# Kernel optimization log

Hardware: AMD Instinct MI355X
Metric: run time of the kernel (lower is better)

Reference implementation:

```python
import jax, jax.numpy as jnp
import numpy as np

EPS = 1e-5

def _ln(x, w, b, axes):
    mu = jnp.mean(x, axis=axes, keepdims=True)
    var = jnp.mean((x - mu) ** 2, axis=axes, keepdims=True)
    return (x - mu) / jnp.sqrt(var + EPS) * w + b

def setup_inputs() -> dict:
    key = jax.random.key(0)
    ks = jax.random.split(key, 6)
    B, L, D, A, H, F = 1, 1024, 512, 32, 8, 2048
    s = 0.02
    return {
        "x": jax.random.normal(ks[0], (B, L, D), jnp.float32),
        "ln0_w": jnp.ones((D,), jnp.float32),
        "ln0_b": jnp.zeros((D,), jnp.float32),
        "ln1_w": jnp.ones((D, H), jnp.float32),
        "ln1_b": jnp.zeros((D, H), jnp.float32),
        "qw": jax.random.normal(ks[1], (D, A * H), jnp.float32) * s,
        "qb": jnp.zeros((A * H,), jnp.float32),
        "kw": jax.random.normal(ks[2], (D, A * H), jnp.float32) * s,
        "kb": jnp.zeros((A * H,), jnp.float32),
        "vw": jax.random.normal(ks[3], (D, D * H), jnp.float32) * s,
        "vb": jnp.zeros((D * H,), jnp.float32),
        "w1": jax.random.normal(ks[4], (D * H, F), jnp.float32) * s,
        "b1": jnp.zeros((F,), jnp.float32),
        "w2": jax.random.normal(ks[5], (F, D), jnp.float32) * s,
        "b2": jnp.zeros((D,), jnp.float32),
    }

def reference(x, ln0_w, ln0_b, ln1_w, ln1_b, qw, qb, kw, kb, vw, vb, w1, b1, w2, b2):
    B, L, D = x.shape
    H = ln1_w.shape[-1]
    _x = _ln(x, ln0_w, ln0_b, -1)
    # q, k: [B, L, d_att, H] with exp(clamp(.)) feature map
    q = jnp.exp(jnp.clip(_x @ qw + qb, -10.0, 10.0)).reshape(B, L, -1, H)
    k = jnp.exp(jnp.clip(_x @ kw + kb, -10.0, 10.0)).reshape(B, L, -1, H)
    # v uses raw x (not layernormed): [B, L, D, H]
    v = (x @ vw + vb).reshape(B, L, D, H)
    # cumulative outer-product KV state: [B, L, d_att, D, H]
    kv = jnp.cumsum(jnp.einsum('blah,bldh->bladh', k, v), axis=1)
    qkv = jnp.einsum('blah,bladh->bldh', q, kv)          # [B, L, D, H]
    den = jnp.einsum('blah,blah->blh', q, jnp.cumsum(k, axis=1))[..., None, :]  # [B, L, 1, H]
    y = x[..., None] + _ln(qkv / den, ln1_w, ln1_b, (-2, -1))  # LN over (D, H) jointly
    y = y.reshape(B, L, D * H)
    h1 = jax.nn.relu(y @ w1 + b1)
    return jax.nn.relu(h1 @ w2 + b2) + x
```

## Files before the change

kernel.cpp:

```cpp
#include <hip/hip_runtime.h>
#include <hip/hip_bf16.h>
#include <math.h>

#define L_SEQ 1024
#define D_DIM 512
#define A_DIM 32
#define H_DIM 8
#define F_DIM 2048
#define AH 256
#define DH 4096
#define NC 16
#define CH 64
#define EPS_LN 1e-5f

typedef __attribute__((ext_vector_type(8))) short short8;
typedef __attribute__((ext_vector_type(4))) short short4v;
typedef __attribute__((ext_vector_type(2))) short short2v;
typedef __attribute__((ext_vector_type(4))) float floatx4;

#define ASYNC_COPY16(gp, lp)                                                     \
    __builtin_amdgcn_global_load_lds(                                            \
        (const __attribute__((address_space(1))) void*)(const void*)(gp),        \
        (__attribute__((address_space(3))) void*)(void*)(lp), 16, 0, 0)

__global__ __launch_bounds__(256) void prep_kernel(const float* __restrict__ x,
                                                   const float* __restrict__ ln0w,
                                                   const float* __restrict__ ln0b,
                                                   const float* __restrict__ ln1w,
                                                   const float* __restrict__ ln1b,
                                                   const float* __restrict__ qw,
                                                   const float* __restrict__ kw,
                                                   const float* __restrict__ vw,
                                                   const float* __restrict__ w1,
                                                   const float* __restrict__ w2,
                                                   __hip_bfloat16* __restrict__ xn,
                                                   __hip_bfloat16* __restrict__ xb,
                                                   __hip_bfloat16* __restrict__ qkwt,
                                                   __hip_bfloat16* __restrict__ vwt,
                                                   __hip_bfloat16* __restrict__ w1t,
                                                   __hip_bfloat16* __restrict__ w2t,
                                                   float* __restrict__ wp,
                                                   float* __restrict__ bp) {
    __shared__ float tt[32][33];
    __shared__ float red[8];
    int bid = blockIdx.x;
    int tid = threadIdx.x;
    if (bid < 1024) {
        int l = bid;
        float v0 = x[l * D_DIM + tid];
        float v1 = x[l * D_DIM + 256 + tid];
        float s = v0 + v1, s2 = v0 * v0 + v1 * v1;
        for (int off = 32; off > 0; off >>= 1) {
            s += __shfl_down(s, off);
            s2 += __shfl_down(s2, off);
        }
        int lane = tid & 63, wid = tid >> 6;
        if (lane == 0) { red[wid] = s; red[4 + wid] = s2; }
        __syncthreads();
        float ts = red[0] + red[1] + red[2] + red[3];
        float t2 = red[4] + red[5] + red[6] + red[7];
        float mu = ts / (float)D_DIM;
        float var = t2 / (float)D_DIM - mu * mu;
        float rs = rsqrtf(var + EPS_LN);
        xn[l * D_DIM + tid]       = (__hip_bfloat16)((v0 - mu) * rs * ln0w[tid] + ln0b[tid]);
        xn[l * D_DIM + 256 + tid] = (__hip_bfloat16)((v1 - mu) * rs * ln0w[256 + tid] + ln0b[256 + tid]);
        xb[l * D_DIM + tid]       = (__hip_bfloat16)v0;
        xb[l * D_DIM + 256 + tid] = (__hip_bfloat16)v1;
        return;
    }
    if (bid == 12544) {
        int e0 = tid * 16;
        float o1[16], o2[16];
#pragma unroll
        for (int j = 0; j < 16; ++j) {
            int ee = e0 + j;
            int pi = ((ee & 511) << 3) | (ee >> 9);
            o1[j] = ln1w[pi];
            o2[j] = ln1b[pi];
        }
#pragma unroll
        for (int j = 0; j < 4; ++j) {
            *(float4*)(wp + e0 + j * 4) = *(float4*)&o1[j * 4];
            *(float4*)(bp + e0 + j * 4) = *(float4*)&o2[j * 4];
        }
        return;
    }
    const float* in;
    __hip_bfloat16* out;
    int R, C, mode = 0, t;
    if (bid < 1152)      { t = bid - 1024;  in = qw; out = qkwt;                      R = 512;  C = 256; }
    else if (bid < 1280) { t = bid - 1152;  in = kw; out = qkwt + (size_t)AH * D_DIM; R = 512;  C = 256; }
    else if (bid < 3328) { t = bid - 1280;  in = vw; out = vwt;  mode = 1;            R = 512;  C = 4096; }
    else if (bid < 11520){ t = bid - 3328;  in = w1; out = w1t;  mode = 2;            R = 4096; C = 2048; }
    else                 { t = bid - 11520; in = w2; out = w2t;                       R = 2048; C = 512; }
    int ctiles = C >> 5;
    int cx = t % ctiles, cy = t / ctiles;
    int r0 = cy * 32, c0 = cx * 32;
    {
        int r_in = tid >> 3, c4 = (tid & 7) * 4;
        int rr = r0 + r_in;
        if (mode == 2) rr = ((rr & 511) << 3) | (rr >> 9);
        float4 v = *(const float4*)(in + (size_t)rr * C + c0 + c4);
        tt[r_in][c4 + 0] = v.x;
        tt[r_in][c4 + 1] = v.y;
        tt[r_in][c4 + 2] = v.z;
        tt[r_in][c4 + 3] = v.w;
    }
    __syncthreads();
    {
        int c_out = tid >> 3, r4 = (tid & 7) * 4;
        int c = c0 + c_out;
        int orow = (mode == 1) ? (((c & 7) << 9) | (c >> 3)) : c;
        __hip_bfloat16 o[4];
#pragma unroll
        for (int j = 0; j < 4; ++j) o[j] = (__hip_bfloat16)tt[r4 + j][c_out];
        *(short4v*)(out + (size_t)orow * R + r0 + r4) = *(short4v*)o;
    }
}

template <int BN>
__device__ __forceinline__ void gemm_core(const __hip_bfloat16* __restrict__ A,
                                          const __hip_bfloat16* __restrict__ Bt,
                                          int K, int bm, int bn, int k_beg, int k_end,
                                          __hip_bfloat16* As, __hip_bfloat16* Bs,
                                          floatx4 (&acc)[2][BN / 32]) {
    constexpr int NT = BN / 32;
    const int tid = threadIdx.x;
    const int w = tid >> 6, lane = tid & 63;
    const int wm = (w >> 1) * 32, wn = (w & 1) * (BN / 2);
    const int quad = lane >> 4, l16 = lane & 15;
    const int srow = tid >> 4, sslot = tid & 15;
    const int scg = sslot ^ srow;
    for (int k0 = k_beg; k0 < k_end; k0 += 128) {
        __syncthreads();
#pragma unroll
        for (int j = 0; j < 4; ++j)
            ASYNC_COPY16(A + (size_t)(bm + j * 16 + srow) * K + k0 + scg * 8,
                         As + j * 2048 + w * 512);
#pragma unroll
        for (int j = 0; j < BN / 16; ++j)
            ASYNC_COPY16(Bt + (size_t)(bn + j * 16 + srow) * K + k0 + scg * 8,
                         Bs + j * 2048 + w * 512);
        __syncthreads();
#pragma unroll
        for (int ks = 0; ks < 4; ++ks) {
            short8 af[2], bfr[NT];
#pragma unroll
            for (int mt = 0; mt < 2; ++mt) {
                int rr = wm + mt * 16 + l16;
                af[mt] = *(const short8*)(As + rr * 128 + (((ks * 4 + quad) ^ (rr & 15)) * 8));
            }
#pragma unroll
            for (int nt = 0; nt < NT; ++nt) {
                int rr = wn + nt * 16 + l16;
                bfr[nt] = *(const short8*)(Bs + rr * 128 + (((ks * 4 + quad) ^ (rr & 15)) * 8));
            }
#pragma unroll
            for (int mt = 0; mt < 2; ++mt)
#pragma unroll
                for (int nt = 0; nt < NT; ++nt)
                    acc[mt][nt] = __builtin_amdgcn_mfma_f32_16x16x32_bf16(
                        af[mt], bfr[nt], acc[mt][nt], 0, 0, 0);
        }
    }
}

__global__ __launch_bounds__(256) void qkv_gemm(const __hip_bfloat16* __restrict__ xn,
                                                const __hip_bfloat16* __restrict__ xb,
                                                const __hip_bfloat16* __restrict__ qkwt,
                                                const __hip_bfloat16* __restrict__ vwt,
                                                const float* __restrict__ qb,
                                                const float* __restrict__ kb,
                                                const float* __restrict__ vb,
                                                __hip_bfloat16* __restrict__ q2,
                                                __hip_bfloat16* __restrict__ k2,
                                                __hip_bfloat16* __restrict__ vT) {
    __shared__ __align__(16) __hip_bfloat16 As[64 * 128];
    __shared__ __align__(16) __hip_bfloat16 Bs[64 * 128];
    const int tid = threadIdx.x;
    const int w = tid >> 6, lane = tid & 63;
    const int wm = (w >> 1) * 32, wn = (w & 1) * 32;
    const int quad = lane >> 4, l16 = lane & 15;
    int bid = blockIdx.x;
    bool isv = bid < 1024;
    const __hip_bfloat16 *A, *Bt;
    int bx, by;
    if (isv) {
        int r = bid >> 3;
        bx = (bid & 7) * 8 + (r & 7);
        by = r >> 3;
        A = xb; Bt = vwt;
    } else {
        int b2 = bid - 1024;
        bx = b2 & 7; by = b2 >> 3;
        A = xn; Bt = qkwt;
    }
    const int bm = by * 64, bn = bx * 64;
    floatx4 acc[2][2];
#pragma unroll
    for (int i = 0; i < 2; ++i)
#pragma unroll
        for (int j = 0; j < 2; ++j) acc[i][j] = (floatx4)0.f;
    gemm_core<64>(A, Bt, D_DIM, bm, bn, 0, D_DIM, As, Bs, acc);
    if (isv) {
        __syncthreads();
        __hip_bfloat16* Ct = As;
#pragma unroll
        for (int mt = 0; mt < 2; ++mt)
#pragma unroll
            for (int nt = 0; nt < 2; ++nt) {
                int col = bn + wn + nt * 16 + l16;
                int bi = ((col & 511) << 3) | (col >> 9);
                float bbv = vb[bi];
                __hip_bfloat16 tmp[4];
#pragma unroll
                for (int r = 0; r < 4; ++r)
                    tmp[r] = (__hip_bfloat16)(acc[mt][nt][r] + bbv);
                *(short4v*)&Ct[(wn + nt * 16 + l16) * 72 + wm + mt * 16 + quad * 4] =
                    *(short4v*)tmp;
            }
        __syncthreads();
        int colloc = tid >> 2, seg = (tid & 3) * 16;
        short8 o0 = *(const short8*)&Ct[colloc * 72 + seg];
        short8 o1 = *(const short8*)&Ct[colloc * 72 + seg + 8];
        *(short8*)(vT + (size_t)(bn + colloc) * 1024 + bm + seg) = o0;
        *(short8*)(vT + (size_t)(bn + colloc) * 1024 + bm + seg + 8) = o1;
    } else {
        __syncthreads();
        __hip_bfloat16* q2t = As;
        bool isq = bn < 256;
        const float* bias = isq ? qb : kb;
        int cb = isq ? bn : bn - 256;
#pragma unroll
        for (int mt = 0; mt < 2; ++mt)
#pragma unroll
            for (int nt = 0; nt < 2; ++nt) {
                int colloc = wn + nt * 16 + l16;
                float bb = bias[cb + colloc];
                int hh = colloc & 7, aa = colloc >> 3;
#pragma unroll
                for (int r = 0; r < 4; ++r) {
                    int rowloc = wm + mt * 16 + quad * 4 + r;
                    float val = expf(fminf(fmaxf(acc[mt][nt][r] + bb, -10.f), 10.f));
                    q2t[((hh * 64 + rowloc) << 3) + aa] = (__hip_bfloat16)val;
                }
            }
        __syncthreads();
        __hip_bfloat16* dst = isq ? q2 : k2;
        int a0 = cb >> 3;
#pragma unroll
        for (int j = 0; j < 2; ++j) {
            int p = tid + j * 256;
            int hh = p >> 6, ll = p & 63;
            short8 o = *(const short8*)&q2t[(hh * 64 + ll) << 3];
            *(short8*)(dst + (size_t)(hh * 1024 + bm + ll) * 32 + a0) = o;
        }
    }
}

__global__ __launch_bounds__(256) void w1_gemm(const __hip_bfloat16* __restrict__ y,
                                               const __hip_bfloat16* __restrict__ w1t,
                                               const float* __restrict__ b1,
                                               __hip_bfloat16* __restrict__ h1) {
    __shared__ __align__(16) __hip_bfloat16 As[64 * 128];
    __shared__ __align__(16) __hip_bfloat16 Bs[32 * 128];
    const int tid = threadIdx.x;
    const int w = tid >> 6, lane = tid & 63;
    const int wm = (w >> 1) * 32, wn = (w & 1) * 16;
    const int quad = lane >> 4, l16 = lane & 15;
    int bid = blockIdx.x;
    int r = bid >> 3;
    int bx = (bid & 7) * 8 + (r & 7);
    int by = r >> 3;
    const int bm = by * 64, bn = bx * 32;
    floatx4 acc[2][1];
    acc[0][0] = (floatx4)0.f;
    acc[1][0] = (floatx4)0.f;
    gemm_core<32>(y, w1t, DH, bm, bn, 0, DH, As, Bs, acc);
    int col = bn + wn + l16;
    float bb = b1[col];
#pragma unroll
    for (int mt = 0; mt < 2; ++mt)
#pragma unroll
        for (int rr = 0; rr < 4; ++rr) {
            int row = bm + wm + mt * 16 + quad * 4 + rr;
            h1[(size_t)row * F_DIM + col] =
                (__hip_bfloat16)fmaxf(acc[mt][0][rr] + bb, 0.f);
        }
}

template <int STRIP>
__global__ __launch_bounds__(256) void gemm_split(const __hip_bfloat16* __restrict__ A,
                                                  const __hip_bfloat16* __restrict__ Bt,
                                                  float* __restrict__ part,
                                                  int M, int N, int K, int Ksub) {
    __shared__ __align__(16) __hip_bfloat16 As[64 * 128];
    __shared__ __align__(16) __hip_bfloat16 Bs[64 * 128];
    const int tid = threadIdx.x;
    const int w = tid >> 6, lane = tid & 63;
    const int wm = (w >> 1) * 32, wn = (w & 1) * 32;
    const int quad = lane >> 4, l16 = lane & 15;
    int bid = blockIdx.x;
    int r = bid >> 3;
    int bx = (bid & 7) * STRIP + (r % STRIP);
    int by = r / STRIP;
    const int bm = by * 64, bn = bx * 64;
    const int kz = blockIdx.z;
    floatx4 acc[2][2];
#pragma unroll
    for (int i = 0; i < 2; ++i)
#pragma unroll
        for (int j = 0; j < 2; ++j) acc[i][j] = (floatx4)0.f;
    gemm_core<64>(A, Bt, K, bm, bn, kz * Ksub, kz * Ksub + Ksub, As, Bs, acc);
#pragma unroll
    for (int mt = 0; mt < 2; ++mt)
#pragma unroll
        for (int nt = 0; nt < 2; ++nt)
#pragma unroll
            for (int rr = 0; rr < 4; ++rr) {
                int row = bm + wm + mt * 16 + quad * 4 + rr;
                int col = bn + wn + nt * 16 + l16;
                part[((size_t)kz * M + row) * N + col] = acc[mt][nt][rr];
            }
}

__global__ __launch_bounds__(256) void w2red(const float* __restrict__ part,
                                             const float* __restrict__ b2,
                                             const float* __restrict__ x,
                                             float* __restrict__ out) {
    size_t e = ((size_t)blockIdx.x * 256 + threadIdx.x) * 4;
    const size_t MN = (size_t)L_SEQ * D_DIM;
    float4 v0 = *(const float4*)(part + e);
    float4 v1 = *(const float4*)(part + MN + e);
    float4 v2 = *(const float4*)(part + 2 * MN + e);
    float4 v3 = *(const float4*)(part + 3 * MN + e);
    float4 bb = *(const float4*)(b2 + (e & 511));
    float4 xx = *(const float4*)(x + e);
    float4 r;
    r.x = fmaxf(v0.x + v1.x + v2.x + v3.x + bb.x, 0.f) + xx.x;
    r.y = fmaxf(v0.y + v1.y + v2.y + v3.y + bb.y, 0.f) + xx.y;
    r.z = fmaxf(v0.z + v1.z + v2.z + v3.z + bb.z, 0.f) + xx.z;
    r.w = fmaxf(v0.w + v1.w + v2.w + v3.w + bb.w, 0.f) + xx.w;
    *(float4*)(out + e) = r;
}

__global__ __launch_bounds__(256) void kvchunk_kernel(const __hip_bfloat16* __restrict__ k2,
                                                      const __hip_bfloat16* __restrict__ vT,
                                                      float* __restrict__ S,
                                                      float* __restrict__ Ka) {
    int c = blockIdx.x, h = blockIdx.y, dq = blockIdx.z;
    int tid = threadIdx.x;
    __shared__ __align__(16) __hip_bfloat16 kaT[32][72];
    __shared__ __align__(16) float St[128][36];
    {
        int l = tid >> 2, a0s = (tid & 3) * 8;
        short8 kv8 = *(const short8*)(k2 + (size_t)(h * 1024 + c * 64 + l) * 32 + a0s);
#pragma unroll
        for (int j = 0; j < 8; ++j)
            kaT[a0s + j][l] = ((const __hip_bfloat16*)&kv8)[j];
    }
    __syncthreads();
    int w = tid >> 6, lane = tid & 63, quad = lane >> 4, l16 = lane & 15;
    floatx4 acc[2][2];
#pragma unroll
    for (int i = 0; i < 2; ++i)
#pragma unroll
        for (int j = 0; j < 2; ++j) acc[i][j] = (floatx4)0.f;
#pragma unroll
    for (int ks = 0; ks < 2; ++ks) {
        short8 af[2], bfr[2];
#pragma unroll
        for (int mt = 0; mt < 2; ++mt)
            af[mt] = *(const short8*)&kaT[mt * 16 + l16][ks * 32 + quad * 8];
#pragma unroll
        for (int nt = 0; nt < 2; ++nt)
            bfr[nt] = *(const short8*)(vT + (size_t)(h * 512 + dq * 128 + w * 32 + nt * 16 + l16) * 1024
                                       + c * 64 + ks * 32 + quad * 8);
#pragma unroll
        for (int mt = 0; mt < 2; ++mt)
#pragma unroll
            for (int nt = 0; nt < 2; ++nt)
                acc[mt][nt] = __builtin_amdgcn_mfma_f32_16x16x32_bf16(
                    af[mt], bfr[nt], acc[mt][nt], 0, 0, 0);
    }
#pragma unroll
    for (int mt = 0; mt < 2; ++mt)
#pragma unroll
        for (int nt = 0; nt < 2; ++nt)
            *(floatx4*)&St[w * 32 + nt * 16 + l16][mt * 16 + quad * 4] = acc[mt][nt];
    __syncthreads();
    int d = tid >> 1, aseg = (tid & 1) * 16;
    float* dst = S + (size_t)((c * 8 + h) * 512 + dq * 128 + d) * 32 + aseg;
    const float* src = &St[d][aseg];
#pragma unroll
    for (int j = 0; j < 4; ++j)
        *(float4*)(dst + j * 4) = *(const float4*)(src + j * 4);
    if (dq == 0 && tid < 32) {
        float s = 0.f;
        for (int l = 0; l < CH; ++l) s += (float)kaT[tid][l];
        Ka[c * AH + tid * 8 + h] = s;
    }
}

__global__ __launch_bounds__(256) void scan_kernel(const float* __restrict__ S,
                                                   const float* __restrict__ Ka,
                                                   __hip_bfloat16* __restrict__ P2,
                                                   float* __restrict__ KaP) {
    size_t j = ((size_t)blockIdx.x * 256 + threadIdx.x) * 2;
    const size_t CS = 8 * 512 * 32;
    float2 run = {0.f, 0.f};
#pragma unroll
    for (int c = 0; c < NC; ++c) {
        __hip_bfloat16 o[2] = {(__hip_bfloat16)run.x, (__hip_bfloat16)run.y};
        *(short2v*)&P2[c * CS + j] = *(short2v*)o;
        float2 sv = *(const float2*)(S + c * CS + j);
        run.x += sv.x; run.y += sv.y;
    }
    if (blockIdx.x == 0) {
        int t = threadIdx.x;
        float rk = 0.f;
        for (int c = 0; c < NC; ++c) {
            KaP[c * AH + t] = rk;
            rk += Ka[c * AH + t];
        }
    }
}

__global__ __launch_bounds__(256) void passC_kernel(const __hip_bfloat16* __restrict__ q2,
                                                    const __hip_bfloat16* __restrict__ k2,
                                                    const __hip_bfloat16* __restrict__ vT,
                                                    const __hip_bfloat16* __restrict__ P2,
                                                    const float* __restrict__ KaP,
                                                    __hip_bfloat16* __restrict__ qkv,
                                                    float* __restrict__ den) {
    int c = blockIdx.x, h = blockIdx.y, dq = blockIdx.z;
    int tid = threadIdx.x;
    __shared__ __align__(16) __hip_bfloat16 Sc[64][72];
    __shared__ float KaPs[32];
    if (dq == 0 && tid < 32) KaPs[tid] = KaP[c * AH + tid * 8 + h];
    int w = tid >> 6, lane = tid & 63, quad = lane >> 4, l16 = lane & 15;
    const size_t qbase = (size_t)(h * 1024 + c * 64) * 32;
    short8 afq = *(const short8*)(q2 + qbase + (w * 16 + l16) * 32 + quad * 8);
    floatx4 sacc[4];
#pragma unroll
    for (int nt = 0; nt < 4; ++nt) sacc[nt] = (floatx4)0.f;
#pragma unroll
    for (int nt = 0; nt < 4; ++nt) {
        short8 bfr = *(const short8*)(k2 + qbase + (nt * 16 + l16) * 32 + quad * 8);
        sacc[nt] = __builtin_amdgcn_mfma_f32_16x16x32_bf16(afq, bfr, sacc[nt], 0, 0, 0);
    }
#pragma unroll
    for (int nt = 0; nt < 4; ++nt)
#pragma unroll
        for (int r = 0; r < 4; ++r) {
            int l = w * 16 + quad * 4 + r;
            int lp = nt * 16 + l16;
            Sc[l][lp] = (__hip_bfloat16)((lp <= l) ? sacc[nt][r] : 0.f);
        }
    __syncthreads();
    if (dq == 0 && tid < 64) {
        int l = tid;
        float s = 0.f;
        for (int lp = 0; lp <= l; ++lp) s += (float)Sc[l][lp];
        const __hip_bfloat16* qp = q2 + qbase + l * 32;
        for (int a = 0; a < A_DIM; ++a) s += (float)qp[a] * KaPs[a];
        den[(c * CH + l) * H_DIM + h] = s;
    }
    floatx4 acc[8];
#pragma unroll
    for (int nt = 0; nt < 8; ++nt) acc[nt] = (floatx4)0.f;
#pragma unroll
    for (int nt = 0; nt < 8; ++nt) {
        short8 pb = *(const short8*)(P2 + ((size_t)((c * 8 + h) * 512 + dq * 128 + nt * 16 + l16)) * 32 + quad * 8);
        acc[nt] = __builtin_amdgcn_mfma_f32_16x16x32_bf16(afq, pb, acc[nt], 0, 0, 0);
    }
#pragma unroll
    for (int ks = 0; ks < 2; ++ks) {
        short8 afs = *(const short8*)&Sc[w * 16 + l16][ks * 32 + quad * 8];
#pragma unroll
        for (int nt = 0; nt < 8; ++nt) {
            short8 bfr = *(const short8*)(vT + (size_t)(h * 512 + dq * 128 + nt * 16 + l16) * 1024
                                          + c * 64 + ks * 32 + quad * 8);
            acc[nt] = __builtin_amdgcn_mfma_f32_16x16x32_bf16(afs, bfr, acc[nt], 0, 0, 0);
        }
    }
#pragma unroll
    for (int nt = 0; nt < 8; ++nt)
#pragma unroll
        for (int r = 0; r < 4; ++r) {
            int l = w * 16 + quad * 4 + r;
            int d = dq * 128 + nt * 16 + l16;
            qkv[(size_t)(c * CH + l) * DH + h * D_DIM + d] = (__hip_bfloat16)acc[nt][r];
        }
}

__global__ __launch_bounds__(256) void ln1_kernel(const __hip_bfloat16* __restrict__ qkv,
                                                  const float* __restrict__ den,
                                                  const float* __restrict__ x,
                                                  const float* __restrict__ wp,
                                                  const float* __restrict__ bp,
                                                  __hip_bfloat16* __restrict__ y) {
    int l = blockIdx.x, tid = threadIdx.x;
    __shared__ float red[8];
    int h = tid >> 5;
    int e0 = tid * 16;
    int d0 = e0 & 511;
    float rden = 1.f / den[l * 8 + h];
    short8 v0 = *(const short8*)(qkv + (size_t)l * DH + e0);
    short8 v1 = *(const short8*)(qkv + (size_t)l * DH + e0 + 8);
    float vals[16];
    float s = 0.f, s2 = 0.f;
#pragma unroll
    for (int j = 0; j < 8; ++j) {
        vals[j] = (float)((const __hip_bfloat16*)&v0)[j] * rden;
        vals[8 + j] = (float)((const __hip_bfloat16*)&v1)[j] * rden;
    }
#pragma unroll
    for (int j = 0; j < 16; ++j) { s += vals[j]; s2 += vals[j] * vals[j]; }
    for (int off = 32; off > 0; off >>= 1) {
        s += __shfl_down(s, off);
        s2 += __shfl_down(s2, off);
    }
    int lane = tid & 63, wid = tid >> 6;
    if (lane == 0) { red[wid] = s; red[4 + wid] = s2; }
    __syncthreads();
    float ts = red[0] + red[1] + red[2] + red[3];
    float t2 = red[4] + red[5] + red[6] + red[7];
    float mu = ts / (float)DH;
    float var = t2 / (float)DH - mu * mu;
    float rs = rsqrtf(var + EPS_LN);
    __hip_bfloat16 o[16];
#pragma unroll
    for (int j4 = 0; j4 < 4; ++j4) {
        float4 xx = *(const float4*)(x + l * D_DIM + d0 + j4 * 4);
        float4 wv = *(const float4*)(wp + e0 + j4 * 4);
        float4 bv = *(const float4*)(bp + e0 + j4 * 4);
        o[j4 * 4 + 0] = (__hip_bfloat16)(xx.x + (vals[j4 * 4 + 0] - mu) * rs * wv.x + bv.x);
        o[j4 * 4 + 1] = (__hip_bfloat16)(xx.y + (vals[j4 * 4 + 1] - mu) * rs * wv.y + bv.y);
        o[j4 * 4 + 2] = (__hip_bfloat16)(xx.z + (vals[j4 * 4 + 2] - mu) * rs * wv.z + bv.z);
        o[j4 * 4 + 3] = (__hip_bfloat16)(xx.w + (vals[j4 * 4 + 3] - mu) * rs * wv.w + bv.w);
    }
    *(short8*)(y + (size_t)l * DH + e0) = *(short8*)&o[0];
    *(short8*)(y + (size_t)l * DH + e0 + 8) = *(short8*)&o[8];
}

extern "C" void kernel_launch(void* const* d_in, const int* in_sizes, int n_in,
                              void* d_out, int out_size, void* d_ws, size_t ws_size,
                              hipStream_t stream) {
    const float* x     = (const float*)d_in[0];
    const float* ln0_w = (const float*)d_in[1];
    const float* ln0_b = (const float*)d_in[2];
    const float* ln1_w = (const float*)d_in[3];
    const float* ln1_b = (const float*)d_in[4];
    const float* qw    = (const float*)d_in[5];
    const float* qb    = (const float*)d_in[6];
    const float* kw    = (const float*)d_in[7];
    const float* kb    = (const float*)d_in[8];
    const float* vw    = (const float*)d_in[9];
    const float* vb    = (const float*)d_in[10];
    const float* w1    = (const float*)d_in[11];
    const float* b1    = (const float*)d_in[12];
    const float* w2    = (const float*)d_in[13];
    const float* b2    = (const float*)d_in[14];
    float* out = (float*)d_out;

    char* ws = (char*)d_ws;
    __hip_bfloat16* xn_bf = (__hip_bfloat16*)(ws + 0);
    __hip_bfloat16* xbf   = (__hip_bfloat16*)(ws + 1048576);
    __hip_bfloat16* qkwt  = (__hip_bfloat16*)(ws + 2097152);
    __hip_bfloat16* vwt   = (__hip_bfloat16*)(ws + 2621440);
    __hip_bfloat16* w1t   = (__hip_bfloat16*)(ws + 6815744);
    __hip_bfloat16* w2t   = (__hip_bfloat16*)(ws + 23592960);
    __hip_bfloat16* q2    = (__hip_bfloat16*)(ws + 25690112);
    __hip_bfloat16* k2    = (__hip_bfloat16*)(ws + 26214400);
    __hip_bfloat16* vT    = (__hip_bfloat16*)(ws + 26738688);
    float* S              = (float*)(ws + 35127296);
    __hip_bfloat16* P2    = (__hip_bfloat16*)(ws + 43515904);
    __hip_bfloat16* qkvb  = (__hip_bfloat16*)(ws + 51904512);
    float* Ka  = (float*)(ws + 60293120);
    float* KaP = (float*)(ws + 60309504);
    float* den = (float*)(ws + 60325888);
    float* wp  = (float*)(ws + 60358656);
    float* bp  = (float*)(ws + 60375040);
    __hip_bfloat16* y  = P2;
    __hip_bfloat16* h1 = (__hip_bfloat16*)S;
    float* w2part = (float*)qkvb;

    prep_kernel<<<12545, 256, 0, stream>>>(x, ln0_w, ln0_b, ln1_w, ln1_b,
                                           qw, kw, vw, w1, w2,
                                           xn_bf, xbf, qkwt, vwt, w1t, w2t, wp, bp);
    qkv_gemm<<<1152, 256, 0, stream>>>(xn_bf, xbf, qkwt, vwt, qb, kb, vb, q2, k2, vT);
    kvchunk_kernel<<<dim3(NC, H_DIM, 4), 256, 0, stream>>>(k2, vT, S, Ka);
    scan_kernel<<<256, 256, 0, stream>>>(S, Ka, P2, KaP);
    passC_kernel<<<dim3(NC, H_DIM, 4), 256, 0, stream>>>(q2, k2, vT, P2, KaP, qkvb, den);
    ln1_kernel<<<L_SEQ, 256, 0, stream>>>(qkvb, den, x, wp, bp, y);
    w1_gemm<<<1024, 256, 0, stream>>>(y, w1t, b1, h1);
    gemm_split<1><<<dim3(128, 1, 4), 256, 0, stream>>>(h1, w2t, w2part,
                                                       L_SEQ, D_DIM, F_DIM, F_DIM / 4);
    w2red<<<(L_SEQ * D_DIM) / 1024, 256, 0, stream>>>(w2part, b2, x, out);

    (void)in_sizes; (void)n_in; (void)out_size; (void)ws_size;
}
```

Measured before the change: 206.7 us.

## Replace split-K W2 GEMM and reduction with single fused 32x64-tile GEMM

The split-K W2 GEMM (4 partial fp32 buffers) and the separate reduction kernel are replaced by one kernel that uses smaller 32x64 tiles over the full K=2048 and applies bias, ReLU and the residual in its epilogue. This drops one launch and the round trip of the fp32 partials (4x1024x512) through global memory. In exchange each block runs a longer K loop, 256 blocks instead of 512, and the loop has no double buffering, so the loads are not overlapped with compute.

```diff
diff --git a/kernel.cpp b/kernel.cpp
--- a/kernel.cpp
+++ b/kernel.cpp
@@ -289,59 +289,56 @@
         }
 }
 
-template <int STRIP>
-__global__ __launch_bounds__(256) void gemm_split(const __hip_bfloat16* __restrict__ A,
-                                                  const __hip_bfloat16* __restrict__ Bt,
-                                                  float* __restrict__ part,
-                                                  int M, int N, int K, int Ksub) {
-    __shared__ __align__(16) __hip_bfloat16 As[64 * 128];
+__global__ __launch_bounds__(256) void w2_gemm(const __hip_bfloat16* __restrict__ h1,
+                                               const __hip_bfloat16* __restrict__ w2t,
+                                               const float* __restrict__ b2,
+                                               const float* __restrict__ x,
+                                               float* __restrict__ out) {
+    __shared__ __align__(16) __hip_bfloat16 As[32 * 128];
     __shared__ __align__(16) __hip_bfloat16 Bs[64 * 128];
     const int tid = threadIdx.x;
     const int w = tid >> 6, lane = tid & 63;
-    const int wm = (w >> 1) * 32, wn = (w & 1) * 32;
+    const int wm = (w >> 1) * 16, wn = (w & 1) * 32;
     const int quad = lane >> 4, l16 = lane & 15;
+    const int srow = tid >> 4, sslot = tid & 15;
+    const int scg = sslot ^ srow;
     int bid = blockIdx.x;
-    int r = bid >> 3;
-    int bx = (bid & 7) * STRIP + (r % STRIP);
-    int by = r / STRIP;
-    const int bm = by * 64, bn = bx * 64;
-    const int kz = blockIdx.z;
-    floatx4 acc[2][2];
-#pragma unroll
-    for (int i = 0; i < 2; ++i)
-#pragma unroll
-        for (int j = 0; j < 2; ++j) acc[i][j] = (floatx4)0.f;
-    gemm_core<64>(A, Bt, K, bm, bn, kz * Ksub, kz * Ksub + Ksub, As, Bs, acc);
-#pragma unroll
-    for (int mt = 0; mt < 2; ++mt)
-#pragma unroll
-        for (int nt = 0; nt < 2; ++nt)
-#pragma unroll
-            for (int rr = 0; rr < 4; ++rr) {
-                int row = bm + wm + mt * 16 + quad * 4 + rr;
-                int col = bn + wn + nt * 16 + l16;
-                part[((size_t)kz * M + row) * N + col] = acc[mt][nt][rr];
+    const int bn = (bid & 7) * 64, bm = (bid >> 3) * 32;
+    floatx4 acc[2];
+    acc[0] = (floatx4)0.f;
+    acc[1] = (floatx4)0.f;
+    for (int k0 = 0; k0 < F_DIM; k0 += 128) {
+        __syncthreads();
+#pragma unroll
+        for (int j = 0; j < 2; ++j)
+            ASYNC_COPY16(h1 + (size_t)(bm + j * 16 + srow) * F_DIM + k0 + scg * 8,
+                         As + j * 2048 + w * 512);
+#pragma unroll
+        for (int j = 0; j < 4; ++j)
+            ASYNC_COPY16(w2t + (size_t)(bn + j * 16 + srow) * F_DIM + k0 + scg * 8,
+                         Bs + j * 2048 + w * 512);
+        __syncthreads();
+#pragma unroll
+        for (int ks = 0; ks < 4; ++ks) {
+            int rra = wm + l16;
+            short8 af = *(const short8*)(As + rra * 128 + (((ks * 4 + quad) ^ (rra & 15)) * 8));
+#pragma unroll
+            for (int nt = 0; nt < 2; ++nt) {
+                int rr = wn + nt * 16 + l16;
+                short8 bfr = *(const short8*)(Bs + rr * 128 + (((ks * 4 + quad) ^ (rr & 15)) * 8));
+                acc[nt] = __builtin_amdgcn_mfma_f32_16x16x32_bf16(af, bfr, acc[nt], 0, 0, 0);
             }
-}
-
-__global__ __launch_bounds__(256) void w2red(const float* __restrict__ part,
-                                             const float* __restrict__ b2,
-                                             const float* __restrict__ x,
-                                             float* __restrict__ out) {
-    size_t e = ((size_t)blockIdx.x * 256 + threadIdx.x) * 4;
-    const size_t MN = (size_t)L_SEQ * D_DIM;
-    float4 v0 = *(const float4*)(part + e);
-    float4 v1 = *(const float4*)(part + MN + e);
-    float4 v2 = *(const float4*)(part + 2 * MN + e);
-    float4 v3 = *(const float4*)(part + 3 * MN + e);
-    float4 bb = *(const float4*)(b2 + (e & 511));
-    float4 xx = *(const float4*)(x + e);
-    float4 r;
-    r.x = fmaxf(v0.x + v1.x + v2.x + v3.x + bb.x, 0.f) + xx.x;
-    r.y = fmaxf(v0.y + v1.y + v2.y + v3.y + bb.y, 0.f) + xx.y;
-    r.z = fmaxf(v0.z + v1.z + v2.z + v3.z + bb.z, 0.f) + xx.z;
-    r.w = fmaxf(v0.w + v1.w + v2.w + v3.w + bb.w, 0.f) + xx.w;
-    *(float4*)(out + e) = r;
+        }
+    }
+#pragma unroll
+    for (int nt = 0; nt < 2; ++nt)
+#pragma unroll
+        for (int r = 0; r < 4; ++r) {
+            int row = bm + wm + quad * 4 + r;
+            int col = bn + wn + nt * 16 + l16;
+            out[(size_t)row * D_DIM + col] =
+                fmaxf(acc[nt][r] + b2[col], 0.f) + x[(size_t)row * D_DIM + col];
+        }
 }
 
 __global__ __launch_bounds__(256) void kvchunk_kernel(const __hip_bfloat16* __restrict__ k2,
@@ -584,7 +581,6 @@
     float* bp  = (float*)(ws + 60375040);
     __hip_bfloat16* y  = P2;
     __hip_bfloat16* h1 = (__hip_bfloat16*)S;
-    float* w2part = (float*)qkvb;
 
     prep_kernel<<<12545, 256, 0, stream>>>(x, ln0_w, ln0_b, ln1_w, ln1_b,
                                            qw, kw, vw, w1, w2,
@@ -595,9 +591,7 @@
     passC_kernel<<<dim3(NC, H_DIM, 4), 256, 0, stream>>>(q2, k2, vT, P2, KaP, qkvb, den);
     ln1_kernel<<<L_SEQ, 256, 0, stream>>>(qkvb, den, x, wp, bp, y);
     w1_gemm<<<1024, 256, 0, stream>>>(y, w1t, b1, h1);
-    gemm_split<1><<<dim3(128, 1, 4), 256, 0, stream>>>(h1, w2t, w2part,
-                                                       L_SEQ, D_DIM, F_DIM, F_DIM / 4);
-    w2red<<<(L_SEQ * D_DIM) / 1024, 256, 0, stream>>>(w2part, b2, x, out);
+    w2_gemm<<<256, 256, 0, stream>>>(h1, w2t, b2, x, out);
 
     (void)in_sizes; (void)n_in; (void)out_size; (void)ws_size;
 }
```

After: 206.1 us. No clear change (-0.3%).
